# Optimization experiments

Measured on AMD Instinct MI355X. Metric: run time of the kernel, lower is better.

## Reference

```python
import jax, jax.numpy as jnp
import numpy as np
from jax import lax


def setup_inputs() -> dict:
    key = jax.random.key(0)
    k1, k2 = jax.random.split(key)
    B, T, D, O = 8, 8192, 512, 512
    x = jax.random.normal(k1, (B, T, D), dtype=jnp.float32)
    # Dense kernel over concat([h_t, state]) -> width 2*D
    W = jax.random.normal(k2, (2 * D, O), dtype=jnp.float32) * (1.0 / np.sqrt(2 * D))
    b = jnp.zeros((O,), dtype=jnp.float32)
    decay = jnp.float32(0.95)
    return {"x": x, "W": W, "b": b, "decay": decay}


def reference(x, W, b, decay):
    # x: [B, T, D]; W: [2D, O]; b: [O]; decay: scalar lambda
    B, T, D = x.shape
    lam = jnp.clip(decay, 0.5, 0.999)  # keras constraint on the decay weight
    h_avg = jnp.mean(x, axis=0)  # [T, D] batch-mean per timestep

    # EMA recurrence: s_t = lam * s_{t-1} + (1 - lam) * h_avg_t, s_{-1} = 0
    def step(s, a):
        s = lam * s + (1.0 - lam) * a
        return s, s

    _, states = lax.scan(step, jnp.zeros((D,), x.dtype), h_avg)  # [T, D]

    # proj(concat([h_t, s_t])) = h_t @ W_h + s_t @ W_s + b (fused, no concat materialized)
    W_h, W_s = W[:D], W[D:]
    out = jnp.einsum('btd,do->bto', x, W_h) + jnp.einsum('td,do->to', states, W_s)[None] + b
    return out  # [B, T, O]
```

## Files before the change

kernel.cpp:

```cpp
#include <hip/hip_runtime.h>
#include <hip/hip_bf16.h>
#include <stdint.h>

#define T_DIM 8192
#define B_DIM 8
#define D_DIM 512
#define O_DIM 512

typedef __attribute__((ext_vector_type(4))) float f32x4;
typedef __attribute__((ext_vector_type(8))) short short8;
typedef __attribute__((ext_vector_type(4))) unsigned short us4;

__device__ __forceinline__ unsigned short f2bf(float f) {
  union { float f; uint32_t u; } v; v.f = f;
  uint32_t u = v.u + 0x7FFFu + ((v.u >> 16) & 1u);
  return (unsigned short)(u >> 16);
}

__device__ __forceinline__ uint32_t cvtpk(float a, float b) {
  uint32_t r;
  asm("v_cvt_pk_bf16_f32 %0, %1, %2" : "=v"(r) : "v"(a), "v"(b));
  return r;
}

__device__ __forceinline__ void gload_lds16(const void* g, void* l) {
  __builtin_amdgcn_global_load_lds(
      (const __attribute__((address_space(1))) void*)g,
      (__attribute__((address_space(3))) void*)l, 16, 0, 0);
}

__device__ __forceinline__ float clip_lam(const float* decay) {
  return fminf(fmaxf(decay[0], 0.5f), 0.999f);
}

__global__ void mean_kernel(const float* __restrict__ x, float* __restrict__ havg) {
  int idx = blockIdx.x * 256 + threadIdx.x;
  const f32x4* x4 = (const f32x4*)x;
  const size_t stride = (size_t)T_DIM * D_DIM / 4;
  f32x4 v[8];
#pragma unroll
  for (int b = 0; b < B_DIM; ++b) v[b] = x4[(size_t)b * stride + idx];
  f32x4 s = ((v[0] + v[1]) + (v[2] + v[3])) + ((v[4] + v[5]) + (v[6] + v[7]));
  s *= 0.125f;
  ((f32x4*)havg)[idx] = s;
}

__global__ void wconv_kernel(const float* __restrict__ W, unsigned short* __restrict__ Wt) {
  __shared__ float tile[64][65];
  int bk = blockIdx.x >> 3;
  int bn = blockIdx.x & 7;
  int tr = threadIdx.x >> 4;
  int tc = threadIdx.x & 15;
#pragma unroll
  for (int i = 0; i < 4; ++i) {
    int row = i * 16 + tr;
    f32x4 v = *(const f32x4*)&W[(size_t)(bk * 64 + row) * O_DIM + bn * 64 + tc * 4];
#pragma unroll
    for (int j = 0; j < 4; ++j) tile[row][tc * 4 + j] = v[j];
  }
  __syncthreads();
#pragma unroll
  for (int i = 0; i < 4; ++i) {
    int nl = i * 16 + tr;
    us4 o;
#pragma unroll
    for (int j = 0; j < 4; ++j) o[j] = f2bf(tile[tc * 4 + j][nl]);
    int kg = bk * 64 + tc * 4;
    int h = kg >> 9;
    int k = kg & 511;
    *(us4*)&Wt[(size_t)h * (512 * 512) + (size_t)(bn * 64 + nl) * 512 + k] = o;
  }
}

#define CHUNK 128
#define NCHUNK (T_DIM / CHUNK)

__global__ void scanA_kernel(float* __restrict__ havg, const float* __restrict__ decay) {
  int chunk = blockIdx.x >> 1;
  int d = ((blockIdx.x & 1) << 8) + threadIdx.x;
  float lam = clip_lam(decay);
  float om = 1.0f - lam;
  size_t base = (size_t)chunk * CHUNK * D_DIM + d;
  float cur[16], nxt[16];
#pragma unroll
  for (int i = 0; i < 16; ++i) cur[i] = havg[base + (size_t)i * D_DIM];
  float s = 0.f;
  for (int blk = 0; blk < 8; ++blk) {
    if (blk < 7) {
#pragma unroll
      for (int i = 0; i < 16; ++i)
        nxt[i] = havg[base + (size_t)((blk + 1) * 16 + i) * D_DIM];
    }
#pragma unroll
    for (int i = 0; i < 16; ++i) {
      s = lam * s + om * cur[i];
      havg[base + (size_t)(blk * 16 + i) * D_DIM] = s;
    }
#pragma unroll
    for (int i = 0; i < 16; ++i) cur[i] = nxt[i];
  }
}

__global__ void scanB_kernel(const float* __restrict__ havg, const float* __restrict__ decay,
                             float* __restrict__ carry) {
  int d = blockIdx.x * 256 + threadIdx.x;
  float lam = clip_lam(decay);
  float l2 = lam * lam;
  float l4 = l2 * l2;
  float l8 = l4 * l4;
  float l16 = l8 * l8;
  float l32 = l16 * l16;
  float l64 = l32 * l32;
  float l128 = l64 * l64;
  float e[NCHUNK];
#pragma unroll
  for (int c = 0; c < NCHUNK; ++c)
    e[c] = havg[((size_t)c * CHUNK + CHUNK - 1) * D_DIM + d];
  float s = 0.f;
#pragma unroll
  for (int c = 0; c < NCHUNK; ++c) {
    s = l128 * s + e[c];
    carry[c * D_DIM + d] = s;
  }
}

__global__ void scanC_kernel(const float* __restrict__ havg, const float* __restrict__ carry,
                             const float* __restrict__ decay, unsigned short* __restrict__ st) {
  int idx = blockIdx.x * 256 + threadIdx.x;
  int t = idx >> 7;
  int d4 = idx & 127;
  int c = t >> 7;
  int k = t & 127;
  float lam = clip_lam(decay);
  float w = exp2f((float)(k + 1) * __log2f(lam));
  f32x4 p = ((const f32x4*)havg)[idx];
  f32x4 cin = {0.f, 0.f, 0.f, 0.f};
  if (c > 0) cin = ((const f32x4*)carry)[(size_t)(c - 1) * 128 + d4];
  us4 o;
#pragma unroll
  for (int j = 0; j < 4; ++j) o[j] = f2bf(p[j] + w * cin[j]);
  ((us4*)st)[idx] = o;
}

template <bool AF32, bool ADD_SBAR>
__global__ __launch_bounds__(256, AF32 ? 3 : 4)
void gemm128(const void* __restrict__ Av, const unsigned short* __restrict__ Bt,
             const float* __restrict__ extra, float* __restrict__ C) {
  constexpr int ABYTES = AF32 ? 16384 : 8192;
  constexpr int BUFB = ABYTES + 8192;
  __shared__ __align__(16) char smem[2][BUFB];

  int nwg = gridDim.x;
  int bid = blockIdx.x;
  int swz = (bid & 7) * (nwg >> 3) + (bid >> 3);
  int tm = swz >> 2, tn = swz & 3;
  int brow = tm << 7, bcol = tn << 7;

  int tid = threadIdx.x;
  int wave = tid >> 6, lane = tid & 63;
  int wr = (wave >> 1) << 6, wc = (wave & 1) << 6;
  const int lr = lane & 15, lkb = lane >> 4;

  const int soct = ((lane & 3) ^ ((lane >> 3) & 3)) << 3;
  const int pm = (lr >> 1) & 3;
  const int kcA = ((lane & 7) ^ (lane >> 3)) << 2;

  const size_t a_base = AF32
      ? (size_t)(brow + (wave << 3) + (lane >> 3)) * 512 + kcA
      : (size_t)(brow + (wave << 4) + (lane >> 2)) * 512 + soct;
  const size_t b_base = (size_t)(bcol + (wave << 4) + (lane >> 2)) * 512 + soct;

  f32x4 acc[4][4];
#pragma unroll
  for (int m = 0; m < 4; ++m)
#pragma unroll
    for (int n = 0; n < 4; ++n) acc[m][n] = (f32x4){0.f, 0.f, 0.f, 0.f};

#define STAGE(buf, kt_)                                                        \
  {                                                                            \
    int k0_ = (kt_) << 5;                                                      \
    if constexpr (AF32) {                                                      \
      const float* Ag = (const float*)Av;                                      \
      _Pragma("unroll")                                                        \
      for (int it = 0; it < 4; ++it)                                           \
        gload_lds16(Ag + a_base + (size_t)(it << 14) + k0_,                    \
                    &smem[buf][(((it << 2) + wave) << 10)]);                   \
    } else {                                                                   \
      const unsigned short* Ag = (const unsigned short*)Av;                    \
      _Pragma("unroll")                                                        \
      for (int it = 0; it < 2; ++it)                                           \
        gload_lds16(Ag + a_base + (size_t)(it << 15) + k0_,                    \
                    &smem[buf][(((it << 2) + wave) << 10)]);                   \
    }                                                                          \
    _Pragma("unroll")                                                          \
    for (int it = 0; it < 2; ++it)                                             \
      gload_lds16(Bt + b_base + (size_t)(it << 15) + k0_,                      \
                  &smem[buf][ABYTES + (((it << 2) + wave) << 10)]);            \
  }

  STAGE(0, 0);

#pragma unroll
  for (int kt = 0; kt < 16; ++kt) {
    const int cur = kt & 1;
    if (kt < 15) {
      STAGE(cur ^ 1, kt + 1);
      if constexpr (AF32)
        asm volatile("s_waitcnt vmcnt(6)" ::: "memory");
      else
        asm volatile("s_waitcnt vmcnt(4)" ::: "memory");
    } else {
      asm volatile("s_waitcnt vmcnt(0)" ::: "memory");
    }
    __builtin_amdgcn_s_barrier();
    __builtin_amdgcn_sched_barrier(0);

    short8 af[4], bfr[4];
    if constexpr (AF32) {
      const float* As = (const float*)&smem[cur][0];
#pragma unroll
      for (int m = 0; m < 4; ++m) {
        int row = wr + (m << 4) + lr;
        int r7 = row & 7;
        int b0 = lkb << 1;
        f32x4 lo = *(const f32x4*)(As + row * 32 + ((b0 ^ r7) << 2));
        f32x4 hi = *(const f32x4*)(As + row * 32 + (((b0 + 1) ^ r7) << 2));
        union { short8 s; uint32_t u[4]; } t;
        t.u[0] = cvtpk(lo[0], lo[1]); t.u[1] = cvtpk(lo[2], lo[3]);
        t.u[2] = cvtpk(hi[0], hi[1]); t.u[3] = cvtpk(hi[2], hi[3]);
        af[m] = t.s;
      }
    } else {
      const unsigned short* As = (const unsigned short*)&smem[cur][0];
#pragma unroll
      for (int m = 0; m < 4; ++m)
        af[m] = *(const short8*)(As + (size_t)(wr + (m << 4) + lr) * 32 + ((lkb ^ pm) << 3));
    }
    const unsigned short* Bs = (const unsigned short*)&smem[cur][ABYTES];
#pragma unroll
    for (int n = 0; n < 4; ++n)
      bfr[n] = *(const short8*)(Bs + (size_t)(wc + (n << 4) + lr) * 32 + ((lkb ^ pm) << 3));

#pragma unroll
    for (int m = 0; m < 4; ++m)
#pragma unroll
      for (int n = 0; n < 4; ++n)
        acc[m][n] = __builtin_amdgcn_mfma_f32_16x16x32_bf16(af[m], bfr[n], acc[m][n], 0, 0, 0);

    __builtin_amdgcn_sched_barrier(0);
    __builtin_amdgcn_s_barrier();
  }
#undef STAGE

  float* tp = (float*)&smem[0][0] + (size_t)wave * 2048;
#pragma unroll
  for (int m = 0; m < 4; ++m) {
#pragma unroll
    for (int n = 0; n < 4; ++n)
#pragma unroll
      for (int j = 0; j < 4; ++j)
        tp[((lkb << 2) + j) * 68 + (n << 4) + lr] = acc[m][n][j];
    __syncthreads();
#pragma unroll
    for (int p = 0; p < 4; ++p) {
      int rl = (p << 2) + (lane >> 4);
      int c0 = (lane & 15) << 2;
      f32x4 v = *(const f32x4*)(tp + rl * 68 + c0);
      int row = brow + wr + (m << 4) + rl;
      int col = bcol + wc + c0;
      f32x4 e;
      if constexpr (ADD_SBAR)
        e = *(const f32x4*)&extra[(size_t)(row & (T_DIM - 1)) * O_DIM + col];
      else
        e = *(const f32x4*)&extra[col];
      v += e;
      *(f32x4*)&C[(size_t)row * O_DIM + col] = v;
    }
    __syncthreads();
  }
}

extern "C" void kernel_launch(void* const* d_in, const int* in_sizes, int n_in,
                              void* d_out, int out_size, void* d_ws, size_t ws_size,
                              hipStream_t stream) {
  (void)in_sizes; (void)n_in; (void)out_size; (void)ws_size;
  const float* x     = (const float*)d_in[0];
  const float* W     = (const float*)d_in[1];
  const float* bias  = (const float*)d_in[2];
  const float* decay = (const float*)d_in[3];
  float* out = (float*)d_out;

  char* ws = (char*)d_ws;
  size_t off = 0;
  float*          havg  = (float*)(ws + off);          off += 16777216;
  unsigned short* st    = (unsigned short*)(ws + off); off += 8388608;
  unsigned short* Wt    = (unsigned short*)(ws + off); off += 1048576;
  float*          sbar  = (float*)(ws + off);          off += 16777216;
  float*          carry = (float*)(ws + off);          off += 131072;

  mean_kernel<<<T_DIM * D_DIM / 4 / 256, 256, 0, stream>>>(x, havg);
  wconv_kernel<<<128, 256, 0, stream>>>(W, Wt);
  scanA_kernel<<<NCHUNK * 2, 256, 0, stream>>>(havg, decay);
  scanB_kernel<<<2, 256, 0, stream>>>(havg, decay, carry);
  scanC_kernel<<<T_DIM * D_DIM / 4 / 256, 256, 0, stream>>>(havg, carry, decay, st);
  gemm128<false, false><<<(T_DIM / 128) * 4, 256, 0, stream>>>(st, Wt + 512 * 512, bias, sbar);
  gemm128<true, true><<<(B_DIM * T_DIM / 128) * 4, 256, 0, stream>>>(x, Wt, sbar, out);
}
```

Baseline: 128.6 us.

## Pre-convert x to bf16 in mean kernel and use bf16-only GEMM

The mean kernel now also writes a bf16 copy of x, already reading all of x to compute the batch mean. The main GEMM then streams bf16 A tiles instead of fp32 tiles and drops the per-tile fp32-to-bf16 conversion, which halves its LDS footprint and allows higher occupancy. The cost is an extra 64 MB bf16 write followed by a re-read, against the old GEMM reading 128 MB of fp32. The k-loop unroll is also reduced to 2.

```diff
diff --git a/kernel.cpp b/kernel.cpp
--- a/kernel.cpp
+++ b/kernel.cpp
@@ -17,12 +17,6 @@
   return (unsigned short)(u >> 16);
 }
 
-__device__ __forceinline__ uint32_t cvtpk(float a, float b) {
-  uint32_t r;
-  asm("v_cvt_pk_bf16_f32 %0, %1, %2" : "=v"(r) : "v"(a), "v"(b));
-  return r;
-}
-
 __device__ __forceinline__ void gload_lds16(const void* g, void* l) {
   __builtin_amdgcn_global_load_lds(
       (const __attribute__((address_space(1))) void*)g,
@@ -33,13 +27,22 @@
   return fminf(fmaxf(decay[0], 0.5f), 0.999f);
 }
 
-__global__ void mean_kernel(const float* __restrict__ x, float* __restrict__ havg) {
+__global__ void mean_cvt_kernel(const float* __restrict__ x, float* __restrict__ havg,
+                                unsigned short* __restrict__ xbf) {
   int idx = blockIdx.x * 256 + threadIdx.x;
   const f32x4* x4 = (const f32x4*)x;
+  us4* xb4 = (us4*)xbf;
   const size_t stride = (size_t)T_DIM * D_DIM / 4;
   f32x4 v[8];
 #pragma unroll
   for (int b = 0; b < B_DIM; ++b) v[b] = x4[(size_t)b * stride + idx];
+  us4 o[8];
+#pragma unroll
+  for (int b = 0; b < B_DIM; ++b)
+#pragma unroll
+    for (int j = 0; j < 4; ++j) o[b][j] = f2bf(v[b][j]);
+#pragma unroll
+  for (int b = 0; b < B_DIM; ++b) xb4[(size_t)b * stride + idx] = o[b];
   f32x4 s = ((v[0] + v[1]) + (v[2] + v[3])) + ((v[4] + v[5]) + (v[6] + v[7]));
   s *= 0.125f;
   ((f32x4*)havg)[idx] = s;
@@ -142,13 +145,11 @@
   ((us4*)st)[idx] = o;
 }
 
-template <bool AF32, bool ADD_SBAR>
-__global__ __launch_bounds__(256, AF32 ? 3 : 4)
-void gemm128(const void* __restrict__ Av, const unsigned short* __restrict__ Bt,
-             const float* __restrict__ extra, float* __restrict__ C) {
-  constexpr int ABYTES = AF32 ? 16384 : 8192;
-  constexpr int BUFB = ABYTES + 8192;
-  __shared__ __align__(16) char smem[2][BUFB];
+template <bool ADD_SBAR>
+__global__ __launch_bounds__(256, 4)
+void gemm128bf(const unsigned short* __restrict__ A, const unsigned short* __restrict__ Bt,
+               const float* __restrict__ extra, float* __restrict__ C) {
+  __shared__ __align__(16) char smem[2][16384];
 
   int nwg = gridDim.x;
   int bid = blockIdx.x;
@@ -163,11 +164,8 @@
 
   const int soct = ((lane & 3) ^ ((lane >> 3) & 3)) << 3;
   const int pm = (lr >> 1) & 3;
-  const int kcA = ((lane & 7) ^ (lane >> 3)) << 2;
-
-  const size_t a_base = AF32
-      ? (size_t)(brow + (wave << 3) + (lane >> 3)) * 512 + kcA
-      : (size_t)(brow + (wave << 4) + (lane >> 2)) * 512 + soct;
+
+  const size_t a_base = (size_t)(brow + (wave << 4) + (lane >> 2)) * 512 + soct;
   const size_t b_base = (size_t)(bcol + (wave << 4) + (lane >> 2)) * 512 + soct;
 
   f32x4 acc[4][4];
@@ -179,64 +177,36 @@
 #define STAGE(buf, kt_)                                                        \
   {                                                                            \
     int k0_ = (kt_) << 5;                                                      \
-    if constexpr (AF32) {                                                      \
-      const float* Ag = (const float*)Av;                                      \
-      _Pragma("unroll")                                                        \
-      for (int it = 0; it < 4; ++it)                                           \
-        gload_lds16(Ag + a_base + (size_t)(it << 14) + k0_,                    \
-                    &smem[buf][(((it << 2) + wave) << 10)]);                   \
-    } else {                                                                   \
-      const unsigned short* Ag = (const unsigned short*)Av;                    \
-      _Pragma("unroll")                                                        \
-      for (int it = 0; it < 2; ++it)                                           \
-        gload_lds16(Ag + a_base + (size_t)(it << 15) + k0_,                    \
-                    &smem[buf][(((it << 2) + wave) << 10)]);                   \
-    }                                                                          \
+    _Pragma("unroll")                                                          \
+    for (int it = 0; it < 2; ++it)                                             \
+      gload_lds16(A + a_base + (size_t)(it << 15) + k0_,                       \
+                  &smem[buf][(((it << 2) + wave) << 10)]);                     \
     _Pragma("unroll")                                                          \
     for (int it = 0; it < 2; ++it)                                             \
       gload_lds16(Bt + b_base + (size_t)(it << 15) + k0_,                      \
-                  &smem[buf][ABYTES + (((it << 2) + wave) << 10)]);            \
+                  &smem[buf][8192 + (((it << 2) + wave) << 10)]);              \
   }
 
   STAGE(0, 0);
 
-#pragma unroll
+#pragma unroll 2
   for (int kt = 0; kt < 16; ++kt) {
     const int cur = kt & 1;
     if (kt < 15) {
       STAGE(cur ^ 1, kt + 1);
-      if constexpr (AF32)
-        asm volatile("s_waitcnt vmcnt(6)" ::: "memory");
-      else
-        asm volatile("s_waitcnt vmcnt(4)" ::: "memory");
+      asm volatile("s_waitcnt vmcnt(4)" ::: "memory");
     } else {
       asm volatile("s_waitcnt vmcnt(0)" ::: "memory");
     }
     __builtin_amdgcn_s_barrier();
     __builtin_amdgcn_sched_barrier(0);
 
+    const unsigned short* As = (const unsigned short*)&smem[cur][0];
+    const unsigned short* Bs = (const unsigned short*)&smem[cur][8192];
     short8 af[4], bfr[4];
-    if constexpr (AF32) {
-      const float* As = (const float*)&smem[cur][0];
-#pragma unroll
-      for (int m = 0; m < 4; ++m) {
-        int row = wr + (m << 4) + lr;
-        int r7 = row & 7;
-        int b0 = lkb << 1;
-        f32x4 lo = *(const f32x4*)(As + row * 32 + ((b0 ^ r7) << 2));
-        f32x4 hi = *(const f32x4*)(As + row * 32 + (((b0 + 1) ^ r7) << 2));
-        union { short8 s; uint32_t u[4]; } t;
-        t.u[0] = cvtpk(lo[0], lo[1]); t.u[1] = cvtpk(lo[2], lo[3]);
-        t.u[2] = cvtpk(hi[0], hi[1]); t.u[3] = cvtpk(hi[2], hi[3]);
-        af[m] = t.s;
-      }
-    } else {
-      const unsigned short* As = (const unsigned short*)&smem[cur][0];
-#pragma unroll
-      for (int m = 0; m < 4; ++m)
-        af[m] = *(const short8*)(As + (size_t)(wr + (m << 4) + lr) * 32 + ((lkb ^ pm) << 3));
-    }
-    const unsigned short* Bs = (const unsigned short*)&smem[cur][ABYTES];
+#pragma unroll
+    for (int m = 0; m < 4; ++m)
+      af[m] = *(const short8*)(As + (size_t)(wr + (m << 4) + lr) * 32 + ((lkb ^ pm) << 3));
 #pragma unroll
     for (int n = 0; n < 4; ++n)
       bfr[n] = *(const short8*)(Bs + (size_t)(wc + (n << 4) + lr) * 32 + ((lkb ^ pm) << 3));
@@ -297,12 +267,13 @@
   unsigned short* Wt    = (unsigned short*)(ws + off); off += 1048576;
   float*          sbar  = (float*)(ws + off);          off += 16777216;
   float*          carry = (float*)(ws + off);          off += 131072;
-
-  mean_kernel<<<T_DIM * D_DIM / 4 / 256, 256, 0, stream>>>(x, havg);
+  unsigned short* xbf   = (unsigned short*)(ws + off); off += (size_t)B_DIM * T_DIM * D_DIM * 2;
+
+  mean_cvt_kernel<<<T_DIM * D_DIM / 4 / 256, 256, 0, stream>>>(x, havg, xbf);
   wconv_kernel<<<128, 256, 0, stream>>>(W, Wt);
   scanA_kernel<<<NCHUNK * 2, 256, 0, stream>>>(havg, decay);
   scanB_kernel<<<2, 256, 0, stream>>>(havg, decay, carry);
   scanC_kernel<<<T_DIM * D_DIM / 4 / 256, 256, 0, stream>>>(havg, carry, decay, st);
-  gemm128<false, false><<<(T_DIM / 128) * 4, 256, 0, stream>>>(st, Wt + 512 * 512, bias, sbar);
-  gemm128<true, true><<<(B_DIM * T_DIM / 128) * 4, 256, 0, stream>>>(x, Wt, sbar, out);
-}
+  gemm128bf<false><<<(T_DIM / 128) * 4, 256, 0, stream>>>(st, Wt + 512 * 512, bias, sbar);
+  gemm128bf<true><<<(B_DIM * T_DIM / 128) * 4, 256, 0, stream>>>(xbf, Wt, sbar, out);
+}
```

New measurement: 136.2 us. 5.9% more time.
